# Kernel tuning notes

Hardware: AMD Instinct MI355X
Metric: run time of the kernel (lower is better)

## Reference

```python
import jax, jax.numpy as jnp
import numpy as np

N, E, H, O = 50000, 640000, 128, 2
N_LAYERS = 3


def setup_inputs() -> dict:
    key = jax.random.key(0)
    ks = jax.random.split(key, 20)
    s = 0.05
    inp = {
        "x": jax.random.normal(ks[0], (N, H), dtype=jnp.float32),
        "edge_index": jax.random.randint(ks[1], (2, E), 0, N, dtype=jnp.int64),
        "edge_type": jax.random.randint(ks[2], (E,), 0, 2, dtype=jnp.int64),
        # msg_sf MLP: Linear(2H->H), ReLU, Linear(H->H)
        "w1_sf": jax.random.normal(ks[3], (2 * H, H), jnp.float32) * s,
        "b1_sf": jnp.zeros((H,), jnp.float32),
        "w2_sf": jax.random.normal(ks[4], (H, H), jnp.float32) * s,
        "b2_sf": jnp.zeros((H,), jnp.float32),
        # msg_fd MLP
        "w1_fd": jax.random.normal(ks[5], (2 * H, H), jnp.float32) * s,
        "b1_fd": jnp.zeros((H,), jnp.float32),
        "w2_fd": jax.random.normal(ks[6], (H, H), jnp.float32) * s,
        "b2_fd": jnp.zeros((H,), jnp.float32),
        # GRUCell gru_h (PyTorch layout: [3H, in] / [3H, H], gate order r,z,n)
        "gru_w_ih": jax.random.normal(ks[7], (3 * H, H), jnp.float32) * s,
        "gru_w_hh": jax.random.normal(ks[8], (3 * H, H), jnp.float32) * s,
        "gru_b_ih": jnp.zeros((3 * H,), jnp.float32),
        "gru_b_hh": jnp.zeros((3 * H,), jnp.float32),
        # readout: Linear(H->H), ReLU, Linear(H->O)
        "wr1": jax.random.normal(ks[9], (H, H), jnp.float32) * s,
        "br1": jnp.zeros((H,), jnp.float32),
        "wr2": jax.random.normal(ks[10], (H, O), jnp.float32) * s,
        "br2": jnp.zeros((O,), jnp.float32),
    }
    return inp


def _mlp(ef, w1, b1, w2, b2):
    return jax.nn.relu(ef @ w1 + b1) @ w2 + b2


def _gru_cell(m, h, w_ih, w_hh, b_ih, b_hh):
    gi = m @ w_ih.T + b_ih  # [N, 3H]
    gh = h @ w_hh.T + b_hh  # [N, 3H]
    r = jax.nn.sigmoid(gi[:, :H] + gh[:, :H])
    z = jax.nn.sigmoid(gi[:, H:2 * H] + gh[:, H:2 * H])
    n = jnp.tanh(gi[:, 2 * H:] + r * gh[:, 2 * H:])
    return (1.0 - z) * n + z * h


def reference(x, edge_index, edge_type,
              w1_sf, b1_sf, w2_sf, b2_sf,
              w1_fd, b1_fd, w2_fd, b2_fd,
              gru_w_ih, gru_w_hh, gru_b_ih, gru_b_hh,
              wr1, br1, wr2, br2):
    src, tgt = edge_index[0], edge_index[1]
    is_sf = (edge_type == 0)[:, None]  # [E, 1]
    h = x
    for _ in range(N_LAYERS):
        # gather source/target node states and concatenate -> [E, 2H]
        ef = jnp.concatenate([h[src], h[tgt]], axis=-1)
        # per-edge message from the edge-type-specific MLP
        m = jnp.where(is_sf,
                      _mlp(ef, w1_sf, b1_sf, w2_sf, b2_sf),
                      _mlp(ef, w1_fd, b1_fd, w2_fd, b2_fd))
        # scatter-add into target nodes
        messages = jax.ops.segment_sum(m, tgt, num_segments=h.shape[0])
        # GRU node update (original's messages.mean(dim=1) is shape-invalid
        # for GRUCell; the runnable interpretation feeds messages directly)
        h = _gru_cell(messages, h, gru_w_ih, gru_w_hh, gru_b_ih, gru_b_hh)
    out = jax.nn.relu(h @ wr1 + br1) @ wr2 + br2
    return jax.nn.softmax(out, axis=1)
```

## Files before the change

kernel.cpp:

```cpp
#include <hip/hip_runtime.h>
#include <hip/hip_bf16.h>


#define NN 50000
#define EE 640000
#define HH 128
#define NBINS (2 * NN)
#define NBLKS 384

typedef __attribute__((ext_vector_type(8))) short short8;
typedef __attribute__((ext_vector_type(4))) float f32x4;

__device__ __forceinline__ unsigned short f2b(float f) {
  __hip_bfloat16 b = __float2bfloat16(f);
  return *reinterpret_cast<unsigned short*>(&b);
}
__device__ __forceinline__ float b2f_lo(unsigned int u) {
  union { unsigned int u; float f; } a; a.u = u << 16; return a.f;
}
__device__ __forceinline__ float b2f_hi(unsigned int u) {
  union { unsigned int u; float f; } a; a.u = u & 0xFFFF0000u; return a.f;
}

__device__ __forceinline__ void gload_lds16(const void* g, void* l) {
  __builtin_amdgcn_global_load_lds((const __attribute__((address_space(1))) void*)g,
                                   (__attribute__((address_space(3))) void*)l, 16, 0, 0);
}

__global__ __launch_bounds__(256) void k_init(const float* __restrict__ x, float* __restrict__ h,
                                              unsigned short* __restrict__ hbf) {
  int i = blockIdx.x * 256 + threadIdx.x;
  float v = x[i];
  h[i] = v;
  hbf[i] = f2b(v);
}

__global__ __launch_bounds__(256) void k_pack(
    const float* __restrict__ w1s, const float* __restrict__ w2s,
    const float* __restrict__ w1f, const float* __restrict__ w2f,
    const float* __restrict__ gwih, const float* __restrict__ gwhh,
    const float* __restrict__ gbih, const float* __restrict__ gbhh,
    unsigned short* __restrict__ pw1s, unsigned short* __restrict__ pw2s,
    unsigned short* __restrict__ pw1f, unsigned short* __restrict__ pw2f,
    unsigned short* __restrict__ pgru, float* __restrict__ bgr) {
  int i = blockIdx.x * 256 + threadIdx.x;
  if (i < 65536) {
    int ty = i >> 15, idx = i & 32767;
    int j = idx & 7, l = (idx >> 3) & 63, kn = idx >> 9;
    int ks = kn & 7, nt = kn >> 3;
    int k = ks * 32 + (l >> 4) * 8 + j, c = nt * 16 + (l & 15);
    const float* w = ty ? w1f : w1s;
    (ty ? pw1f : pw1s)[idx] = f2b(w[k * 128 + c]);
  } else if (i < 98304) {
    int i2 = i - 65536;
    int ty = i2 >> 14, idx = i2 & 16383;
    int j = idx & 7, l = (idx >> 3) & 63, kn = idx >> 9;
    int ks = kn & 3, nt = kn >> 2;
    int k = ks * 32 + (l >> 4) * 8 + j, c = nt * 16 + (l & 15);
    const float* w = ty ? w2f : w2s;
    (ty ? pw2f : pw2s)[idx] = f2b(w[k * 128 + c]);
  } else if (i < 98304 + 131072) {
    int idx = i - 98304;
    int j = idx & 7, l = (idx >> 3) & 63, kc = idx >> 9;
    int ks = kc & 7, ct = kc >> 3;
    int k = ks * 32 + (l >> 4) * 8 + j, c = ct * 16 + (l & 15);
    float v;
    if (c < 256)      v = (k < 128) ? gwih[c * 128 + k] : gwhh[c * 128 + (k - 128)];
    else if (c < 384) v = (k < 128) ? gwih[c * 128 + k] : 0.f;
    else              v = (k >= 128) ? gwhh[(c - 128) * 128 + (k - 128)] : 0.f;
    pgru[idx] = f2b(v);
  } else if (i < 98304 + 131072 + 512) {
    int j = i - (98304 + 131072);
    float v;
    if (j < 256)      v = gbih[j] + gbhh[j];
    else if (j < 384) v = gbih[j];
    else              v = gbhh[j - 128];
    bgr[j] = v;
  }
}

__global__ __launch_bounds__(256) void k_hist(const int* __restrict__ ei, const int* __restrict__ et,
                                              int* __restrict__ hist) {
  int e = blockIdx.x * 256 + threadIdx.x;
  int g = ei[EE + e];
  int ty = et[e];
  atomicAdd(&hist[ty * NN + g], 1);
}

__global__ __launch_bounds__(1024) void k_scan1(const int* __restrict__ hist, int* __restrict__ base,
                                                int* __restrict__ bsum) {
  __shared__ int sh[1024];
  int t = threadIdx.x;
  int i = blockIdx.x * 1024 + t;
  int v = (i < NBINS) ? hist[i] : 0;
  sh[t] = v;
  __syncthreads();
  for (int o = 1; o < 1024; o <<= 1) {
    int xv = (t >= o) ? sh[t - o] : 0;
    __syncthreads();
    sh[t] += xv;
    __syncthreads();
  }
  if (i < NBINS) base[i] = sh[t] - v;
  if (t == 1023) bsum[blockIdx.x] = sh[t];
}

__global__ __launch_bounds__(128) void k_scan2(int* __restrict__ bsum) {
  __shared__ int sh[128];
  int t = threadIdx.x;
  int v = (t < 98) ? bsum[t] : 0;
  sh[t] = v;
  __syncthreads();
  for (int o = 1; o < 128; o <<= 1) {
    int xv = (t >= o) ? sh[t - o] : 0;
    __syncthreads();
    sh[t] += xv;
    __syncthreads();
  }
  if (t < 98) bsum[t] = sh[t] - v;
}

__global__ __launch_bounds__(1024) void k_scan3(const int* __restrict__ bsum, int* __restrict__ base,
                                                int* __restrict__ cnt) {
  int i = blockIdx.x * 1024 + threadIdx.x;
  if (i < NBINS) {
    int b = base[i] + bsum[blockIdx.x];
    base[i] = b;
    if (i == NN) cnt[0] = b;
  }
}

__global__ __launch_bounds__(256) void k_scatter(const int* __restrict__ ei, const int* __restrict__ et,
                                                 int* __restrict__ woff, int* __restrict__ ssrc,
                                                 int* __restrict__ stgt) {
  int e = blockIdx.x * 256 + threadIdx.x;
  int s = ei[e], g = ei[EE + e], ty = et[e];
  int pos = atomicAdd(&woff[ty * NN + g], 1);
  ssrc[pos] = s;
  stgt[pos] = g;
}

__global__ __launch_bounds__(256, 2) void k_edge(
    const unsigned short* __restrict__ hbf,
    const int* __restrict__ ssrc, const int* __restrict__ stgt,
    const unsigned short* __restrict__ pw1s, const unsigned short* __restrict__ pw2s,
    const unsigned short* __restrict__ pw1f, const unsigned short* __restrict__ pw2f,
    const float* __restrict__ b1s, const float* __restrict__ b2s,
    const float* __restrict__ b1f, const float* __restrict__ b2f,
    float* __restrict__ msg, const int* __restrict__ cnt) {
  __shared__ char efA[16384];
  __shared__ char efB[16384];
  __shared__ char mC[17408];
  __shared__ int idxbuf[2][2][64];
  const int tid = threadIdx.x, l = tid & 63, w = tid >> 6;
  const int c0 = cnt[0];
  const int type = (blockIdx.x >= NBLKS) ? 1 : 0;
  const int bsub = type ? (blockIdx.x - NBLKS) : blockIdx.x;
  const int lo = type ? c0 : 0;
  const int hi = type ? EE : c0;
  const int ntile = (hi - lo + 63) >> 6;
  if (bsub >= ntile) return;
  const int nblk = 1 + (ntile - 1 - bsub) / NBLKS;
  const unsigned short* pw1 = type ? pw1f : pw1s;
  const unsigned short* pw2 = type ? pw2f : pw2s;
  const float* b1 = type ? b1f : b1s;
  const float* b2 = type ? b2f : b2s;

  short8 wb1[2][8], wb2[2][4];
#pragma unroll
  for (int q = 0; q < 2; q++) {
    int nt = 2 * w + q;
#pragma unroll
    for (int ks = 0; ks < 8; ks++)
      wb1[q][ks] = *(const short8*)(pw1 + ((nt * 8 + ks) * 64 + l) * 8);
#pragma unroll
    for (int ks = 0; ks < 4; ks++)
      wb2[q][ks] = *(const short8*)(pw2 + ((nt * 4 + ks) * 64 + l) * 8);
  }
  float b1v[2], b2v[2];
  b1v[0] = b1[(2 * w) * 16 + (l & 15)];
  b1v[1] = b1[(2 * w + 1) * 16 + (l & 15)];
  b2v[0] = b2[(2 * w) * 16 + (l & 15)];
  b2v[1] = b2[(2 * w + 1) * 16 + (l & 15)];

  auto issue_gathers = [&](int slot) {
#pragma unroll
    for (int i = 0; i < 4; i++) {
      int r = w * 16 + i * 4 + (l >> 4);
      int j = (l & 15) ^ (r & 7);
      int nodeS = idxbuf[slot][0][r];
      gload_lds16(hbf + (size_t)nodeS * HH + j * 8, efA + w * 4096 + i * 1024);
      int nodeT = idxbuf[slot][1][r];
      if (nodeT < 0) nodeT = 0;
      gload_lds16(hbf + (size_t)nodeT * HH + j * 8, efB + w * 4096 + i * 1024);
    }
  };

  {
    int p0 = lo + bsub * 64 + (tid & 63);
    if (tid < 64) {
      int v = (p0 < hi) ? ssrc[p0] : 0;
      if (v < 0) v = 0;
      idxbuf[0][0][tid] = v;
    } else if (tid < 128) {
      int v = (p0 < hi) ? stgt[p0] : -1;
      idxbuf[0][1][tid & 63] = v;
    }
  }
  int ridx = (tid < 64) ? 0 : -1;
  {
    int p1 = lo + (bsub + NBLKS) * 64 + (tid & 63);
    if (tid < 128 && p1 < hi) ridx = (tid < 64) ? ssrc[p1] : stgt[p1];
  }
  asm volatile("s_waitcnt lgkmcnt(0)" ::: "memory");
  __builtin_amdgcn_s_barrier();
  issue_gathers(0);

  f32x4 zero4 = {0.f, 0.f, 0.f, 0.f};
  for (int k = 0; k < nblk; k++) {
    const int cur = k & 1, nxt = cur ^ 1;
    asm volatile("s_waitcnt vmcnt(0)" ::: "memory");
    __builtin_amdgcn_sched_barrier(0);
    __builtin_amdgcn_s_barrier();

    f32x4 acc[4][2];
#pragma unroll
    for (int mt = 0; mt < 4; mt++)
#pragma unroll
      for (int q = 0; q < 2; q++) acc[mt][q] = zero4;
    __builtin_amdgcn_s_setprio(1);
#pragma unroll
    for (int ks = 0; ks < 8; ks++) {
      const char* ef = (ks < 4) ? efA : efB;
      int ko = (ks & 3) * 64;
      short8 a[4];
#pragma unroll
      for (int mt = 0; mt < 4; mt++) {
        int row = mt * 16 + (l & 15);
        a[mt] = *(const short8*)(ef + row * 256 + ((ko + (l >> 4) * 16) ^ ((row & 7) << 4)));
      }
#pragma unroll
      for (int mt = 0; mt < 4; mt++)
#pragma unroll
        for (int q = 0; q < 2; q++)
          acc[mt][q] = __builtin_amdgcn_mfma_f32_16x16x32_bf16(a[mt], wb1[q][ks], acc[mt][q], 0, 0, 0);
    }
    __builtin_amdgcn_s_setprio(0);
    if (tid < 128) {
      int v = ridx;
      if (tid < 64 && v < 0) v = 0;
      idxbuf[nxt][tid >= 64 ? 1 : 0][tid & 63] = v;
    }
    {
      int p2 = lo + (bsub + (k + 2) * NBLKS) * 64 + (tid & 63);
      ridx = (tid < 64) ? 0 : -1;
      if (tid < 128 && p2 < hi) ridx = (tid < 64) ? ssrc[p2] : stgt[p2];
    }
#pragma unroll
    for (int mt = 0; mt < 4; mt++)
#pragma unroll
      for (int q = 0; q < 2; q++) {
        int col = (2 * w + q) * 16 + (l & 15);
#pragma unroll
        for (int r = 0; r < 4; r++) {
          int row = mt * 16 + (l >> 4) * 4 + r;
          float v = acc[mt][q][r] + b1v[q];
          v = v > 0.f ? v : 0.f;
          *(unsigned short*)(mC + row * 256 + ((col * 2) ^ ((row & 7) << 4))) = f2b(v);
        }
      }
    asm volatile("s_waitcnt lgkmcnt(0)" ::: "memory");
    __builtin_amdgcn_s_barrier();

    if (k + 1 < nblk) issue_gathers(nxt);
    f32x4 acc2[4][2];
#pragma unroll
    for (int mt = 0; mt < 4; mt++)
#pragma unroll
      for (int q = 0; q < 2; q++) acc2[mt][q] = zero4;
    __builtin_amdgcn_s_setprio(1);
#pragma unroll
    for (int ks = 0; ks < 4; ks++) {
      short8 a[4];
#pragma unroll
      for (int mt = 0; mt < 4; mt++) {
        int row = mt * 16 + (l & 15);
        a[mt] = *(const short8*)(mC + row * 256 + ((ks * 64 + (l >> 4) * 16) ^ ((row & 7) << 4)));
      }
#pragma unroll
      for (int mt = 0; mt < 4; mt++)
#pragma unroll
        for (int q = 0; q < 2; q++)
          acc2[mt][q] = __builtin_amdgcn_mfma_f32_16x16x32_bf16(a[mt], wb2[q][ks], acc2[mt][q], 0, 0, 0);
    }
    __builtin_amdgcn_s_setprio(0);
    __builtin_amdgcn_s_barrier();

#pragma unroll
    for (int mt = 0; mt < 4; mt++)
#pragma unroll
      for (int q = 0; q < 2; q++) {
        int col = (2 * w + q) * 16 + (l & 15);
        int e0 = mt * 16 + (l >> 4) * 4;
        f32x4 v = acc2[mt][q];
        unsigned int u0 = (unsigned int)f2b(v.x + b2v[q]) | ((unsigned int)f2b(v.y + b2v[q]) << 16);
        unsigned int u1 = (unsigned int)f2b(v.z + b2v[q]) | ((unsigned int)f2b(v.w + b2v[q]) << 16);
        *(unsigned int*)(mC + col * 132 + e0 * 2) = u0;
        *(unsigned int*)(mC + col * 132 + e0 * 2 + 4) = u1;
      }
    asm volatile("s_waitcnt lgkmcnt(0)" ::: "memory");
    __builtin_amdgcn_s_barrier();

    {
      int f = tid & 127, grp = tid >> 7;
      float accum = 0.f;
      int curg = idxbuf[cur][1][grp * 32];
#pragma unroll
      for (int jj = 0; jj < 8; jj++) {
        int4 tg = *(const int4*)&idxbuf[cur][1][grp * 32 + jj * 4];
        unsigned int m0 = *(const unsigned int*)(mC + f * 132 + (grp * 32 + jj * 4) * 2);
        unsigned int m1 = *(const unsigned int*)(mC + f * 132 + (grp * 32 + jj * 4) * 2 + 4);
        float vv[4];
        vv[0] = b2f_lo(m0); vv[1] = b2f_hi(m0);
        vv[2] = b2f_lo(m1); vv[3] = b2f_hi(m1);
        int gg[4] = {tg.x, tg.y, tg.z, tg.w};
#pragma unroll
        for (int r = 0; r < 4; r++) {
          if (gg[r] != curg) {
            if (curg >= 0) atomicAdd(&msg[(size_t)curg * HH + f], accum);
            accum = 0.f;
            curg = gg[r];
          }
          accum += vv[r];
        }
      }
      if (curg >= 0) atomicAdd(&msg[(size_t)curg * HH + f], accum);
    }
  }
}

__global__ __launch_bounds__(256) void k_gru(
    const float* __restrict__ msg, const unsigned short* __restrict__ pgru,
    const float* __restrict__ bgr, float* __restrict__ h, unsigned short* __restrict__ hbf) {
  __shared__ char amh[64 * 512];
  int tid = threadIdx.x, l = tid & 63, w = tid >> 6;
  int n0 = blockIdx.x * 64;
#pragma unroll
  for (int i = 0; i < 8; i++) {
    int c = tid + i * 256;
    int r = c >> 5, cc = c & 31;
    int node = n0 + r; if (node > NN - 1) node = NN - 1;
    float4 v = *((const float4*)(msg + (size_t)node * HH) + cc);
    uint2 u;
    u.x = (unsigned int)f2b(v.x) | ((unsigned int)f2b(v.y) << 16);
    u.y = (unsigned int)f2b(v.z) | ((unsigned int)f2b(v.w) << 16);
    *(uint2*)(amh + r * 512 + ((cc * 8) ^ ((r & 7) << 4))) = u;
  }
#pragma unroll
  for (int i = 0; i < 4; i++) {
    int c = tid + i * 256;
    int r = c >> 4, cc = c & 15;
    int node = n0 + r; if (node > NN - 1) node = NN - 1;
    int4 v = *((const int4*)(hbf + (size_t)node * HH) + cc);
    *(int4*)(amh + r * 512 + ((256 + cc * 16) ^ ((r & 7) << 4))) = v;
  }
  __syncthreads();

  f32x4 zero4 = {0.f, 0.f, 0.f, 0.f};
  f32x4 acc[4][8];
#pragma unroll
  for (int mt = 0; mt < 4; mt++)
#pragma unroll
    for (int t = 0; t < 8; t++) acc[mt][t] = zero4;
#pragma unroll
  for (int ks = 0; ks < 8; ks++) {
    short8 a[4];
#pragma unroll
    for (int mt = 0; mt < 4; mt++) {
      int row = mt * 16 + (l & 15);
      a[mt] = *(const short8*)(amh + row * 512 + ((ks * 64 + (l >> 4) * 16) ^ ((row & 7) << 4)));
    }
#pragma unroll
    for (int t = 0; t < 8; t++) {
      int ct = w + 4 * t;
      short8 bf = *(const short8*)(pgru + ((ct * 8 + ks) * 64 + l) * 8);
#pragma unroll
      for (int mt = 0; mt < 4; mt++)
        acc[mt][t] = __builtin_amdgcn_mfma_f32_16x16x32_bf16(a[mt], bf, acc[mt][t], 0, 0, 0);
    }
  }

#pragma unroll
  for (int tt = 0; tt < 2; tt++) {
    int ct = w + 4 * tt;
    int j = ct * 16 + (l & 15);
    float br = bgr[j], bz = bgr[128 + j], bgi = bgr[256 + j], bgh = bgr[384 + j];
#pragma unroll
    for (int mt = 0; mt < 4; mt++) {
#pragma unroll
      for (int r = 0; r < 4; r++) {
        int row = mt * 16 + (l >> 4) * 4 + r;
        int node = n0 + row;
        if (node < NN) {
          float hold = h[(size_t)node * HH + j];
          float ur = acc[mt][tt][r] + br;
          float uz = acc[mt][tt + 2][r] + bz;
          float gi = acc[mt][tt + 4][r] + bgi;
          float gh = acc[mt][tt + 6][r] + bgh;
          float rr = 1.f / (1.f + __expf(-ur));
          float zz = 1.f / (1.f + __expf(-uz));
          float xx = gi + rr * gh;
          xx = fminf(fmaxf(xx, -15.f), 15.f);
          float ex = __expf(2.f * xx);
          float nn2 = (ex - 1.f) / (ex + 1.f);
          float hn = (1.f - zz) * nn2 + zz * hold;
          h[(size_t)node * HH + j] = hn;
          hbf[(size_t)node * HH + j] = f2b(hn);
        }
      }
    }
  }
}

__global__ __launch_bounds__(256) void k_read(const float* __restrict__ h,
                                              const float* __restrict__ wr1, const float* __restrict__ br1,
                                              const float* __restrict__ wr2, const float* __restrict__ br2,
                                              float* __restrict__ out) {
  __shared__ float sh[16][128];
  int tid = threadIdx.x, l = tid & 63, w = tid >> 6;
  int nb = blockIdx.x * 16;
#pragma unroll
  for (int i = 0; i < 8; i++) {
    int c = tid + i * 256;
    int r = c >> 7, k = c & 127;
    int node = nb + r; if (node > NN - 1) node = NN - 1;
    sh[r][k] = h[(size_t)node * HH + k];
  }
  __syncthreads();
  float a1[4] = {0.f, 0.f, 0.f, 0.f}, a2[4] = {0.f, 0.f, 0.f, 0.f};
  for (int k = 0; k < 128; k++) {
    float w1a = wr1[k * 128 + l];
    float w1b = wr1[k * 128 + l + 64];
#pragma unroll
    for (int n = 0; n < 4; n++) {
      float hv = sh[w * 4 + n][k];
      a1[n] += hv * w1a;
      a2[n] += hv * w1b;
    }
  }
  float bra = br1[l], brb = br1[l + 64];
  float w20 = wr2[l * 2 + 0], w21 = wr2[l * 2 + 1];
  float w20b = wr2[(l + 64) * 2 + 0], w21b = wr2[(l + 64) * 2 + 1];
#pragma unroll
  for (int n = 0; n < 4; n++) {
    float h1 = fmaxf(a1[n] + bra, 0.f), h2 = fmaxf(a2[n] + brb, 0.f);
    float l0 = h1 * w20 + h2 * w20b;
    float l1 = h1 * w21 + h2 * w21b;
#pragma unroll
    for (int o = 32; o > 0; o >>= 1) {
      l0 += __shfl_xor(l0, o);
      l1 += __shfl_xor(l1, o);
    }
    if (l == 0) {
      int node = nb + w * 4 + n;
      if (node < NN) {
        l0 += br2[0];
        l1 += br2[1];
        float mx = fmaxf(l0, l1);
        float e0 = __expf(l0 - mx), e1 = __expf(l1 - mx);
        float s = e0 + e1;
        out[node * 2 + 0] = e0 / s;
        out[node * 2 + 1] = e1 / s;
      }
    }
  }
}

extern "C" void kernel_launch(void* const* d_in, const int* in_sizes, int n_in,
                              void* d_out, int out_size, void* d_ws, size_t ws_size,
                              hipStream_t stream) {
  const float* x    = (const float*)d_in[0];
  const int*   ei   = (const int*)d_in[1];
  const int*   et   = (const int*)d_in[2];
  const float* w1s  = (const float*)d_in[3];
  const float* b1s  = (const float*)d_in[4];
  const float* w2s  = (const float*)d_in[5];
  const float* b2s  = (const float*)d_in[6];
  const float* w1f  = (const float*)d_in[7];
  const float* b1f  = (const float*)d_in[8];
  const float* w2f  = (const float*)d_in[9];
  const float* b2f  = (const float*)d_in[10];
  const float* gwih = (const float*)d_in[11];
  const float* gwhh = (const float*)d_in[12];
  const float* gbih = (const float*)d_in[13];
  const float* gbhh = (const float*)d_in[14];
  const float* wr1  = (const float*)d_in[15];
  const float* br1  = (const float*)d_in[16];
  const float* wr2  = (const float*)d_in[17];
  const float* br2  = (const float*)d_in[18];
  float* out = (float*)d_out;
  (void)in_sizes; (void)n_in; (void)out_size; (void)ws_size;

  char* p = (char*)d_ws;
  size_t off = 0;
  auto alloc = [&](size_t sz) {
    char* r = p + off;
    off = (off + sz + 255) & ~(size_t)255;
    return r;
  };
  float* h             = (float*)alloc((size_t)NN * HH * 4);
  unsigned short* hbf  = (unsigned short*)alloc((size_t)NN * HH * 2);
  float* msg           = (float*)alloc((size_t)NN * HH * 4);
  int* ssrc            = (int*)alloc((size_t)EE * 4);
  int* stgt            = (int*)alloc((size_t)EE * 4);
  int* hist            = (int*)alloc((size_t)NBINS * 4);
  int* base            = (int*)alloc((size_t)NBINS * 4);
  int* woff            = (int*)alloc((size_t)NBINS * 4);
  int* bsum            = (int*)alloc(128 * 4);
  int* cnt             = (int*)alloc(16);
  unsigned short* pw1s = (unsigned short*)alloc(32768 * 2);
  unsigned short* pw2s = (unsigned short*)alloc(16384 * 2);
  unsigned short* pw1f = (unsigned short*)alloc(32768 * 2);
  unsigned short* pw2f = (unsigned short*)alloc(16384 * 2);
  unsigned short* pgru = (unsigned short*)alloc(131072 * 2);
  float* bgr           = (float*)alloc(512 * 4);

  hipMemsetAsync(hist, 0, (size_t)NBINS * 4, stream);
  k_init<<<NN * HH / 256, 256, 0, stream>>>(x, h, hbf);
  k_pack<<<898, 256, 0, stream>>>(w1s, w2s, w1f, w2f, gwih, gwhh, gbih, gbhh,
                                  pw1s, pw2s, pw1f, pw2f, pgru, bgr);
  k_hist<<<EE / 256, 256, 0, stream>>>(ei, et, hist);
  k_scan1<<<98, 1024, 0, stream>>>(hist, base, bsum);
  k_scan2<<<1, 128, 0, stream>>>(bsum);
  k_scan3<<<98, 1024, 0, stream>>>(bsum, base, cnt);
  hipMemcpyAsync(woff, base, (size_t)NBINS * 4, hipMemcpyDeviceToDevice, stream);
  k_scatter<<<EE / 256, 256, 0, stream>>>(ei, et, woff, ssrc, stgt);

  for (int layer = 0; layer < 3; layer++) {
    hipMemsetAsync(msg, 0, (size_t)NN * HH * 4, stream);
    k_edge<<<2 * NBLKS, 256, 0, stream>>>(hbf, ssrc, stgt, pw1s, pw2s, pw1f, pw2f,
                                          b1s, b2s, b1f, b2f, msg, cnt);
    k_gru<<<(NN + 63) / 64, 256, 0, stream>>>(msg, pgru, bgr, h, hbf);
  }
  k_read<<<NN / 16, 256, 0, stream>>>(h, wr1, br1, wr2, br2, out);
}
```

Measured before the change: 656.0 us.

## Replace persistent pipelined edge kernel with one-tile-per-block direct gathers; fuse msg zeroing

The edge kernel previously ran a fixed grid of persistent blocks. Each block kept its MLP weights in registers and double-buffered node-feature gathers into LDS with async global-to-LDS loads. It now launches one block per 64-edge tile. Each block loads its MFMA A-fragments straight from global memory into registers and reloads weight fragments from global at every k-step. This drops 32KB of LDS per block and the manual pipelining, aiming at higher occupancy and less synchronisation, but it loses cross-tile overlap and weight reuse. Separately, the per-layer memset of the message buffer is removed: k_gru now zeroes each message row after reading it, with a single memset before the layer loop.

```diff
diff --git a/kernel.cpp b/kernel.cpp
--- a/kernel.cpp
+++ b/kernel.cpp
@@ -6,7 +6,7 @@
 #define EE 640000
 #define HH 128
 #define NBINS (2 * NN)
-#define NBLKS 384
+#define NTILES (EE / 64)
 
 typedef __attribute__((ext_vector_type(8))) short short8;
 typedef __attribute__((ext_vector_type(4))) float f32x4;
@@ -20,11 +20,6 @@
 }
 __device__ __forceinline__ float b2f_hi(unsigned int u) {
   union { unsigned int u; float f; } a; a.u = u & 0xFFFF0000u; return a.f;
-}
-
-__device__ __forceinline__ void gload_lds16(const void* g, void* l) {
-  __builtin_amdgcn_global_load_lds((const __attribute__((address_space(1))) void*)g,
-                                   (__attribute__((address_space(3))) void*)l, 16, 0, 0);
 }
 
 __global__ __launch_bounds__(256) void k_init(const float* __restrict__ x, float* __restrict__ h,
@@ -148,209 +143,166 @@
     const float* __restrict__ b1s, const float* __restrict__ b2s,
     const float* __restrict__ b1f, const float* __restrict__ b2f,
     float* __restrict__ msg, const int* __restrict__ cnt) {
-  __shared__ char efA[16384];
-  __shared__ char efB[16384];
   __shared__ char mC[17408];
-  __shared__ int idxbuf[2][2][64];
+  __shared__ int idxS[64];
+  __shared__ int idxT[64];
   const int tid = threadIdx.x, l = tid & 63, w = tid >> 6;
   const int c0 = cnt[0];
-  const int type = (blockIdx.x >= NBLKS) ? 1 : 0;
-  const int bsub = type ? (blockIdx.x - NBLKS) : blockIdx.x;
+  const int bid = blockIdx.x;
+  const int type = (bid >= NTILES) ? 1 : 0;
+  const int tb = type ? (bid - NTILES) : bid;
   const int lo = type ? c0 : 0;
   const int hi = type ? EE : c0;
-  const int ntile = (hi - lo + 63) >> 6;
-  if (bsub >= ntile) return;
-  const int nblk = 1 + (ntile - 1 - bsub) / NBLKS;
+  const int start = lo + tb * 64;
+  if (start >= hi) return;
   const unsigned short* pw1 = type ? pw1f : pw1s;
   const unsigned short* pw2 = type ? pw2f : pw2s;
   const float* b1 = type ? b1f : b1s;
   const float* b2 = type ? b2f : b2s;
 
-  short8 wb1[2][8], wb2[2][4];
-#pragma unroll
-  for (int q = 0; q < 2; q++) {
-    int nt = 2 * w + q;
-#pragma unroll
-    for (int ks = 0; ks < 8; ks++)
-      wb1[q][ks] = *(const short8*)(pw1 + ((nt * 8 + ks) * 64 + l) * 8);
-#pragma unroll
-    for (int ks = 0; ks < 4; ks++)
-      wb2[q][ks] = *(const short8*)(pw2 + ((nt * 4 + ks) * 64 + l) * 8);
-  }
+  if (tid < 64) {
+    int pp = start + tid;
+    int v = (pp < hi) ? ssrc[pp] : 0;
+    idxS[tid] = (v < 0) ? 0 : v;
+  } else if (tid < 128) {
+    int pp = start + (tid & 63);
+    idxT[tid & 63] = (pp < hi) ? stgt[pp] : -1;
+  }
+  __syncthreads();
+
+  int nS[4], nT[4];
+#pragma unroll
+  for (int mt = 0; mt < 4; mt++) {
+    nS[mt] = idxS[mt * 16 + (l & 15)];
+    int g = idxT[mt * 16 + (l & 15)];
+    nT[mt] = (g < 0) ? 0 : g;
+  }
+
   float b1v[2], b2v[2];
   b1v[0] = b1[(2 * w) * 16 + (l & 15)];
   b1v[1] = b1[(2 * w + 1) * 16 + (l & 15)];
   b2v[0] = b2[(2 * w) * 16 + (l & 15)];
   b2v[1] = b2[(2 * w + 1) * 16 + (l & 15)];
 
-  auto issue_gathers = [&](int slot) {
-#pragma unroll
-    for (int i = 0; i < 4; i++) {
-      int r = w * 16 + i * 4 + (l >> 4);
-      int j = (l & 15) ^ (r & 7);
-      int nodeS = idxbuf[slot][0][r];
-      gload_lds16(hbf + (size_t)nodeS * HH + j * 8, efA + w * 4096 + i * 1024);
-      int nodeT = idxbuf[slot][1][r];
-      if (nodeT < 0) nodeT = 0;
-      gload_lds16(hbf + (size_t)nodeT * HH + j * 8, efB + w * 4096 + i * 1024);
-    }
-  };
+  f32x4 zero4 = {0.f, 0.f, 0.f, 0.f};
+  f32x4 acc[4][2];
+#pragma unroll
+  for (int mt = 0; mt < 4; mt++)
+#pragma unroll
+    for (int q = 0; q < 2; q++) acc[mt][q] = zero4;
+  const int koff = (l >> 4) * 8;
+#pragma unroll
+  for (int ks = 0; ks < 8; ks++) {
+    short8 a[4];
+#pragma unroll
+    for (int mt = 0; mt < 4; mt++) {
+      int node = (ks < 4) ? nS[mt] : nT[mt];
+      a[mt] = *(const short8*)(hbf + (size_t)node * HH + (ks & 3) * 32 + koff);
+    }
+    short8 wb0 = *(const short8*)(pw1 + (((2 * w) * 8 + ks) * 64 + l) * 8);
+    short8 wb1 = *(const short8*)(pw1 + (((2 * w + 1) * 8 + ks) * 64 + l) * 8);
+#pragma unroll
+    for (int mt = 0; mt < 4; mt++) {
+      acc[mt][0] = __builtin_amdgcn_mfma_f32_16x16x32_bf16(a[mt], wb0, acc[mt][0], 0, 0, 0);
+      acc[mt][1] = __builtin_amdgcn_mfma_f32_16x16x32_bf16(a[mt], wb1, acc[mt][1], 0, 0, 0);
+    }
+  }
+
+#pragma unroll
+  for (int mt = 0; mt < 4; mt++)
+#pragma unroll
+    for (int q = 0; q < 2; q++) {
+      int col = (2 * w + q) * 16 + (l & 15);
+#pragma unroll
+      for (int r = 0; r < 4; r++) {
+        int row = mt * 16 + (l >> 4) * 4 + r;
+        float v = acc[mt][q][r] + b1v[q];
+        v = v > 0.f ? v : 0.f;
+        *(unsigned short*)(mC + row * 256 + ((col * 2) ^ ((row & 7) << 4))) = f2b(v);
+      }
+    }
+  __syncthreads();
+
+  f32x4 acc2[4][2];
+#pragma unroll
+  for (int mt = 0; mt < 4; mt++)
+#pragma unroll
+    for (int q = 0; q < 2; q++) acc2[mt][q] = zero4;
+#pragma unroll
+  for (int ks = 0; ks < 4; ks++) {
+    short8 a[4];
+#pragma unroll
+    for (int mt = 0; mt < 4; mt++) {
+      int row = mt * 16 + (l & 15);
+      a[mt] = *(const short8*)(mC + row * 256 + ((ks * 64 + (l >> 4) * 16) ^ ((row & 7) << 4)));
+    }
+    short8 wb0 = *(const short8*)(pw2 + (((2 * w) * 4 + ks) * 64 + l) * 8);
+    short8 wb1 = *(const short8*)(pw2 + (((2 * w + 1) * 4 + ks) * 64 + l) * 8);
+#pragma unroll
+    for (int mt = 0; mt < 4; mt++) {
+      acc2[mt][0] = __builtin_amdgcn_mfma_f32_16x16x32_bf16(a[mt], wb0, acc2[mt][0], 0, 0, 0);
+      acc2[mt][1] = __builtin_amdgcn_mfma_f32_16x16x32_bf16(a[mt], wb1, acc2[mt][1], 0, 0, 0);
+    }
+  }
+  __syncthreads();
+
+#pragma unroll
+  for (int mt = 0; mt < 4; mt++)
+#pragma unroll
+    for (int q = 0; q < 2; q++) {
+      int col = (2 * w + q) * 16 + (l & 15);
+      int e0 = mt * 16 + (l >> 4) * 4;
+      f32x4 v = acc2[mt][q];
+      unsigned int u0 = (unsigned int)f2b(v.x + b2v[q]) | ((unsigned int)f2b(v.y + b2v[q]) << 16);
+      unsigned int u1 = (unsigned int)f2b(v.z + b2v[q]) | ((unsigned int)f2b(v.w + b2v[q]) << 16);
+      *(unsigned int*)(mC + col * 132 + e0 * 2) = u0;
+      *(unsigned int*)(mC + col * 132 + e0 * 2 + 4) = u1;
+    }
+  __syncthreads();
 
   {
-    int p0 = lo + bsub * 64 + (tid & 63);
-    if (tid < 64) {
-      int v = (p0 < hi) ? ssrc[p0] : 0;
-      if (v < 0) v = 0;
-      idxbuf[0][0][tid] = v;
-    } else if (tid < 128) {
-      int v = (p0 < hi) ? stgt[p0] : -1;
-      idxbuf[0][1][tid & 63] = v;
-    }
-  }
-  int ridx = (tid < 64) ? 0 : -1;
-  {
-    int p1 = lo + (bsub + NBLKS) * 64 + (tid & 63);
-    if (tid < 128 && p1 < hi) ridx = (tid < 64) ? ssrc[p1] : stgt[p1];
-  }
-  asm volatile("s_waitcnt lgkmcnt(0)" ::: "memory");
-  __builtin_amdgcn_s_barrier();
-  issue_gathers(0);
-
-  f32x4 zero4 = {0.f, 0.f, 0.f, 0.f};
-  for (int k = 0; k < nblk; k++) {
-    const int cur = k & 1, nxt = cur ^ 1;
-    asm volatile("s_waitcnt vmcnt(0)" ::: "memory");
-    __builtin_amdgcn_sched_barrier(0);
-    __builtin_amdgcn_s_barrier();
-
-    f32x4 acc[4][2];
-#pragma unroll
-    for (int mt = 0; mt < 4; mt++)
-#pragma unroll
-      for (int q = 0; q < 2; q++) acc[mt][q] = zero4;
-    __builtin_amdgcn_s_setprio(1);
-#pragma unroll
-    for (int ks = 0; ks < 8; ks++) {
-      const char* ef = (ks < 4) ? efA : efB;
-      int ko = (ks & 3) * 64;
-      short8 a[4];
-#pragma unroll
-      for (int mt = 0; mt < 4; mt++) {
-        int row = mt * 16 + (l & 15);
-        a[mt] = *(const short8*)(ef + row * 256 + ((ko + (l >> 4) * 16) ^ ((row & 7) << 4)));
+    int f = tid & 127, grp = tid >> 7;
+    float accum = 0.f;
+    int curg = idxT[grp * 32];
+#pragma unroll
+    for (int jj = 0; jj < 8; jj++) {
+      int4 tg = *(const int4*)&idxT[grp * 32 + jj * 4];
+      unsigned int m0 = *(const unsigned int*)(mC + f * 132 + (grp * 32 + jj * 4) * 2);
+      unsigned int m1 = *(const unsigned int*)(mC + f * 132 + (grp * 32 + jj * 4) * 2 + 4);
+      float vv[4];
+      vv[0] = b2f_lo(m0); vv[1] = b2f_hi(m0);
+      vv[2] = b2f_lo(m1); vv[3] = b2f_hi(m1);
+      int gg[4] = {tg.x, tg.y, tg.z, tg.w};
+#pragma unroll
+      for (int r = 0; r < 4; r++) {
+        if (gg[r] != curg) {
+          if (curg >= 0) atomicAdd(&msg[(size_t)curg * HH + f], accum);
+          accum = 0.f;
+          curg = gg[r];
+        }
+        accum += vv[r];
       }
-#pragma unroll
-      for (int mt = 0; mt < 4; mt++)
-#pragma unroll
-        for (int q = 0; q < 2; q++)
-          acc[mt][q] = __builtin_amdgcn_mfma_f32_16x16x32_bf16(a[mt], wb1[q][ks], acc[mt][q], 0, 0, 0);
-    }
-    __builtin_amdgcn_s_setprio(0);
-    if (tid < 128) {
-      int v = ridx;
-      if (tid < 64 && v < 0) v = 0;
-      idxbuf[nxt][tid >= 64 ? 1 : 0][tid & 63] = v;
-    }
-    {
-      int p2 = lo + (bsub + (k + 2) * NBLKS) * 64 + (tid & 63);
-      ridx = (tid < 64) ? 0 : -1;
-      if (tid < 128 && p2 < hi) ridx = (tid < 64) ? ssrc[p2] : stgt[p2];
-    }
-#pragma unroll
-    for (int mt = 0; mt < 4; mt++)
-#pragma unroll
-      for (int q = 0; q < 2; q++) {
-        int col = (2 * w + q) * 16 + (l & 15);
-#pragma unroll
-        for (int r = 0; r < 4; r++) {
-          int row = mt * 16 + (l >> 4) * 4 + r;
-          float v = acc[mt][q][r] + b1v[q];
-          v = v > 0.f ? v : 0.f;
-          *(unsigned short*)(mC + row * 256 + ((col * 2) ^ ((row & 7) << 4))) = f2b(v);
-        }
-      }
-    asm volatile("s_waitcnt lgkmcnt(0)" ::: "memory");
-    __builtin_amdgcn_s_barrier();
-
-    if (k + 1 < nblk) issue_gathers(nxt);
-    f32x4 acc2[4][2];
-#pragma unroll
-    for (int mt = 0; mt < 4; mt++)
-#pragma unroll
-      for (int q = 0; q < 2; q++) acc2[mt][q] = zero4;
-    __builtin_amdgcn_s_setprio(1);
-#pragma unroll
-    for (int ks = 0; ks < 4; ks++) {
-      short8 a[4];
-#pragma unroll
-      for (int mt = 0; mt < 4; mt++) {
-        int row = mt * 16 + (l & 15);
-        a[mt] = *(const short8*)(mC + row * 256 + ((ks * 64 + (l >> 4) * 16) ^ ((row & 7) << 4)));
-      }
-#pragma unroll
-      for (int mt = 0; mt < 4; mt++)
-#pragma unroll
-        for (int q = 0; q < 2; q++)
-          acc2[mt][q] = __builtin_amdgcn_mfma_f32_16x16x32_bf16(a[mt], wb2[q][ks], acc2[mt][q], 0, 0, 0);
-    }
-    __builtin_amdgcn_s_setprio(0);
-    __builtin_amdgcn_s_barrier();
-
-#pragma unroll
-    for (int mt = 0; mt < 4; mt++)
-#pragma unroll
-      for (int q = 0; q < 2; q++) {
-        int col = (2 * w + q) * 16 + (l & 15);
-        int e0 = mt * 16 + (l >> 4) * 4;
-        f32x4 v = acc2[mt][q];
-        unsigned int u0 = (unsigned int)f2b(v.x + b2v[q]) | ((unsigned int)f2b(v.y + b2v[q]) << 16);
-        unsigned int u1 = (unsigned int)f2b(v.z + b2v[q]) | ((unsigned int)f2b(v.w + b2v[q]) << 16);
-        *(unsigned int*)(mC + col * 132 + e0 * 2) = u0;
-        *(unsigned int*)(mC + col * 132 + e0 * 2 + 4) = u1;
-      }
-    asm volatile("s_waitcnt lgkmcnt(0)" ::: "memory");
-    __builtin_amdgcn_s_barrier();
-
-    {
-      int f = tid & 127, grp = tid >> 7;
-      float accum = 0.f;
-      int curg = idxbuf[cur][1][grp * 32];
-#pragma unroll
-      for (int jj = 0; jj < 8; jj++) {
-        int4 tg = *(const int4*)&idxbuf[cur][1][grp * 32 + jj * 4];
-        unsigned int m0 = *(const unsigned int*)(mC + f * 132 + (grp * 32 + jj * 4) * 2);
-        unsigned int m1 = *(const unsigned int*)(mC + f * 132 + (grp * 32 + jj * 4) * 2 + 4);
-        float vv[4];
-        vv[0] = b2f_lo(m0); vv[1] = b2f_hi(m0);
-        vv[2] = b2f_lo(m1); vv[3] = b2f_hi(m1);
-        int gg[4] = {tg.x, tg.y, tg.z, tg.w};
-#pragma unroll
-        for (int r = 0; r < 4; r++) {
-          if (gg[r] != curg) {
-            if (curg >= 0) atomicAdd(&msg[(size_t)curg * HH + f], accum);
-            accum = 0.f;
-            curg = gg[r];
-          }
-          accum += vv[r];
-        }
-      }
-      if (curg >= 0) atomicAdd(&msg[(size_t)curg * HH + f], accum);
-    }
+    }
+    if (curg >= 0) atomicAdd(&msg[(size_t)curg * HH + f], accum);
   }
 }
 
 __global__ __launch_bounds__(256) void k_gru(
     const float* __restrict__ msg, const unsigned short* __restrict__ pgru,
-    const float* __restrict__ bgr, float* __restrict__ h, unsigned short* __restrict__ hbf) {
+    const float* __restrict__ bgr, float* __restrict__ h, unsigned short* __restrict__ hbf,
+    float* __restrict__ msgw, int dz) {
   __shared__ char amh[64 * 512];
   int tid = threadIdx.x, l = tid & 63, w = tid >> 6;
   int n0 = blockIdx.x * 64;
+  f32x4 zero4 = {0.f, 0.f, 0.f, 0.f};
 #pragma unroll
   for (int i = 0; i < 8; i++) {
     int c = tid + i * 256;
     int r = c >> 5, cc = c & 31;
-    int node = n0 + r; if (node > NN - 1) node = NN - 1;
+    int node0 = n0 + r;
+    int node = node0 > NN - 1 ? NN - 1 : node0;
     float4 v = *((const float4*)(msg + (size_t)node * HH) + cc);
+    if (dz && node0 < NN) *((f32x4*)(msgw + (size_t)node0 * HH) + cc) = zero4;
     uint2 u;
     u.x = (unsigned int)f2b(v.x) | ((unsigned int)f2b(v.y) << 16);
     u.y = (unsigned int)f2b(v.z) | ((unsigned int)f2b(v.w) << 16);
@@ -366,7 +318,6 @@
   }
   __syncthreads();
 
-  f32x4 zero4 = {0.f, 0.f, 0.f, 0.f};
   f32x4 acc[4][8];
 #pragma unroll
   for (int mt = 0; mt < 4; mt++)
@@ -535,12 +486,12 @@
   k_scan3<<<98, 1024, 0, stream>>>(bsum, base, cnt);
   hipMemcpyAsync(woff, base, (size_t)NBINS * 4, hipMemcpyDeviceToDevice, stream);
   k_scatter<<<EE / 256, 256, 0, stream>>>(ei, et, woff, ssrc, stgt);
+  hipMemsetAsync(msg, 0, (size_t)NN * HH * 4, stream);
 
   for (int layer = 0; layer < 3; layer++) {
-    hipMemsetAsync(msg, 0, (size_t)NN * HH * 4, stream);
-    k_edge<<<2 * NBLKS, 256, 0, stream>>>(hbf, ssrc, stgt, pw1s, pw2s, pw1f, pw2f,
-                                          b1s, b2s, b1f, b2f, msg, cnt);
-    k_gru<<<(NN + 63) / 64, 256, 0, stream>>>(msg, pgru, bgr, h, hbf);
+    k_edge<<<2 * NTILES, 256, 0, stream>>>(hbf, ssrc, stgt, pw1s, pw2s, pw1f, pw2f,
+                                           b1s, b2s, b1f, b2f, msg, cnt);
+    k_gru<<<(NN + 63) / 64, 256, 0, stream>>>(msg, pgru, bgr, h, hbf, msg, layer < 2 ? 1 : 0);
   }
   k_read<<<NN / 16, 256, 0, stream>>>(h, wr1, br1, wr2, br2, out);
 }
```

After: 737.1 us. +12.4%, slower.
